# Kernel optimization log

Measured on AMD Instinct MI355X. Metric: run time of the kernel, lower is better.

## Reference

```python
import jax, jax.numpy as jnp
import numpy as np

G = 4          # deformable groups (from offset_and_mask_dim = 3*4*3*3)
K = 9          # 3x3 kernel points
GN_GROUPS = 16 # GroupNorm groups as in DyHead


def conv2d(x, w, stride=1, pad=1, groups=1):
    return jax.lax.conv_general_dilated(
        x, w, (stride, stride), [(pad, pad), (pad, pad)],
        dimension_numbers=('NCHW', 'OIHW', 'NCHW'),
        feature_group_count=groups)


def dw_conv(x, w, scale, bias):
    # YOLO Conv with g=in_channels: depthwise 3x3 + folded BN + SiLU
    C = x.shape[1]
    y = conv2d(x, w, groups=C)
    y = y * scale[None, :, None, None] + bias[None, :, None, None]
    return y * jax.nn.sigmoid(y)


def offset_mask_conv(x, w, b):
    # Conv2d(C, 108, 3, padding=1, groups=4)
    return conv2d(x, w, groups=G) + b[None, :, None, None]


def split_offset_mask(om, use_softmax):
    # om: (N,108,H,W) -> offset (N,H,W,G,K,2) in pixels (dy,dx), mask (N,H,W,G,K)
    N, _, H, W = om.shape
    om = om.transpose(0, 2, 3, 1)
    offset = om[..., :2 * G * K].reshape(N, H, W, G, K, 2)
    m = om[..., 2 * G * K:].reshape(N, H, W, G, K)
    mask = jax.nn.softmax(m, axis=-1) if use_softmax else jax.nn.sigmoid(m)
    return offset, mask


def group_norm(x, gamma, beta, eps=1e-5):
    N, C, H, W = x.shape
    xg = x.reshape(N, GN_GROUPS, C // GN_GROUPS, H, W)
    mu = xg.mean((2, 3, 4), keepdims=True)
    var = xg.var((2, 3, 4), keepdims=True)
    xg = (xg - mu) * jax.lax.rsqrt(var + eps)
    return xg.reshape(N, C, H, W) * gamma[None, :, None, None] + beta[None, :, None, None]


def dcnv3_sample(x, offset, mask, stride):
    # DCNv3 core: group-wise deformable 3x3 bilinear sampling, zero padding.
    # x: (N,C,H,W); offset: (N,Ho,Wo,G,K,2); mask: (N,Ho,Wo,G,K) -> (N,C,Ho,Wo)
    N, C, H, W = x.shape
    Cg = C // G
    Ho, Wo = offset.shape[1], offset.shape[2]
    xg = x.transpose(0, 2, 3, 1).reshape(N, H, W, G, Cg)
    kk = jnp.arange(3, dtype=x.dtype) - 1.0
    ky = jnp.repeat(kk, 3)  # (9,)
    kx = jnp.tile(kk, 3)
    base_y = (jnp.arange(Ho, dtype=x.dtype) * stride)[None, :, None, None, None]
    base_x = (jnp.arange(Wo, dtype=x.dtype) * stride)[None, None, :, None, None]
    py = base_y + ky + offset[..., 0]   # (N,Ho,Wo,G,K)
    px = base_x + kx + offset[..., 1]
    y0 = jnp.floor(py)
    x0 = jnp.floor(px)
    wy = py - y0
    wx = px - x0
    y0i = y0.astype(jnp.int32)
    x0i = x0.astype(jnp.int32)
    n_idx = jnp.arange(N)[:, None, None, None, None]
    g_idx = jnp.arange(G)[None, None, None, :, None]
    acc = jnp.zeros((N, Ho, Wo, G, Cg), x.dtype)
    for dy in (0, 1):
        for dx in (0, 1):
            yi = y0i + dy
            xi = x0i + dx
            w = (wy if dy else 1.0 - wy) * (wx if dx else 1.0 - wx)
            valid = (yi >= 0) & (yi < H) & (xi >= 0) & (xi < W)
            w = w * valid.astype(x.dtype) * mask
            v = xg[n_idx, jnp.clip(yi, 0, H - 1), jnp.clip(xi, 0, W - 1), g_idx]  # (N,Ho,Wo,G,K,Cg)
            acc = acc + jnp.einsum('nhwgk,nhwgkc->nhwgc', w, v)
    return acc.reshape(N, Ho, Wo, C).transpose(0, 3, 1, 2)


def up_bilinear_ac(x, Ho, Wo):
    # bilinear, align_corners=True
    N, C, H, W = x.shape
    def coords(out, size):
        c = jnp.arange(out, dtype=jnp.float32) * ((size - 1) / max(out - 1, 1))
        i0 = jnp.floor(c).astype(jnp.int32)
        i1 = jnp.minimum(i0 + 1, size - 1)
        return i0, i1, (c - i0).astype(x.dtype)
    y0, y1, wy = coords(Ho, H)
    xc0, xc1, wx = coords(Wo, W)
    t = x[:, :, y0, :] * (1.0 - wy)[None, None, :, None] + x[:, :, y1, :] * wy[None, None, :, None]
    return t[:, :, :, xc0] * (1.0 - wx) + t[:, :, :, xc1] * wx


def scale_attn(f, w, b):
    # AdaptiveAvgPool2d(1) -> Conv 1x1 (C->1) -> ReLU -> HSigmoid(bias=3, divisor=6)
    y = f.mean((2, 3))                      # (N,C)
    a = jax.nn.relu(y @ w.T + b)            # (N,1)
    a = jnp.clip((a + 3.0) / 6.0, 0.0, 1.0)
    return f * a[:, :, None, None]


def dyrelu(f, w1, b1_, w2, b2_):
    # DyReLU with K2=True, use_bias=True, lambda_a=2, init_a=[1,0], init_b=[0,0]
    y = f.mean((2, 3))                      # (N,C)
    h = jax.nn.relu(y @ w1.T + b1_)
    z = jnp.clip(h @ w2.T + b2_ + 3.0, 0.0, 6.0) / 6.0  # h_sigmoid
    a1, b1, a2, b2 = jnp.split(z, 4, axis=1)
    a1 = (a1 - 0.5) * 2.0 + 1.0
    a2 = (a2 - 0.5) * 2.0
    b1 = b1 - 0.5
    b2 = b2 - 0.5
    bc = lambda t: t[:, :, None, None]
    return jnp.maximum(f * bc(a1) + bc(b1), f * bc(a2) + bc(b2))


def _forward(x0, x1, x2,
             dw_w_h, dw_s_h, dw_b_h, dw_w_m, dw_s_m, dw_b_m, dw_w_l, dw_s_l, dw_b_l,
             off_w, off_b,
             gn_g_h, gn_b_h, gn_g_m, gn_b_m, gn_g_l, gn_b_l,
             sa_w, sa_b, fc1_w, fc1_b, fc2_w, fc2_b):
    xs = [x0, x1, x2]
    outs = []
    for lvl in range(3):
        x = xs[lvl]
        mid_ = dw_conv(x, dw_w_m, dw_s_m, dw_b_m)
        off, msk = split_offset_mask(offset_mask_conv(mid_, off_w, off_b), use_softmax=False)
        mid_feat = group_norm(dcnv3_sample(x, off, msk, 1), gn_g_m, gn_b_m)
        sum_feat = scale_attn(mid_feat, sa_w, sa_b)
        n_lvls = 1
        if lvl > 0:
            xl = xs[lvl - 1]
            low_ = dw_conv(xl, dw_w_l, dw_s_l, dw_b_l)
            off, msk = split_offset_mask(offset_mask_conv(low_, off_w, off_b), use_softmax=True)
            off = off[:, ::2, ::2]   # stride-2 output grid
            msk = msk[:, ::2, ::2]
            low_feat = group_norm(dcnv3_sample(xl, off, msk, 2), gn_g_l, gn_b_l)
            sum_feat = sum_feat + scale_attn(low_feat, sa_w, sa_b)
            n_lvls += 1
        if lvl < 2:
            xh = xs[lvl + 1]
            high_ = dw_conv(xh, dw_w_h, dw_s_h, dw_b_h)
            off, msk = split_offset_mask(offset_mask_conv(high_, off_w, off_b), use_softmax=True)
            high_feat = group_norm(dcnv3_sample(xh, off, msk, 1), gn_g_h, gn_b_h)
            high_feat = up_bilinear_ac(high_feat, x.shape[2], x.shape[3])
            sum_feat = sum_feat + scale_attn(high_feat, sa_w, sa_b)
            n_lvls += 1
        outs.append(dyrelu(sum_feat / n_lvls, fc1_w, fc1_b, fc2_w, fc2_b))
    return tuple(outs)


def setup_inputs() -> dict:
    key = jax.random.key(0)
    ks = jax.random.split(key, 32)
    N, C = 4, 256
    f32 = jnp.float32
    nrm = lambda k, shape, s=1.0: jax.random.normal(k, shape, f32) * s
    inp = {
        'x0': nrm(ks[0], (N, C, 80, 80)),
        'x1': nrm(ks[1], (N, C, 40, 40)),
        'x2': nrm(ks[2], (N, C, 20, 20)),
        'dw_w_h': nrm(ks[3], (C, 1, 3, 3), 0.1),
        'dw_s_h': 1.0 + nrm(ks[4], (C,), 0.1),
        'dw_b_h': nrm(ks[5], (C,), 0.1),
        'dw_w_m': nrm(ks[6], (C, 1, 3, 3), 0.1),
        'dw_s_m': 1.0 + nrm(ks[7], (C,), 0.1),
        'dw_b_m': nrm(ks[8], (C,), 0.1),
        'dw_w_l': nrm(ks[9], (C, 1, 3, 3), 0.1),
        'dw_s_l': 1.0 + nrm(ks[10], (C,), 0.1),
        'dw_b_l': nrm(ks[11], (C,), 0.1),
        'off_w': nrm(ks[12], (108, C // G, 3, 3), 0.1),
        'off_b': nrm(ks[13], (108,), 0.1),
        'gn_g_h': 1.0 + nrm(ks[14], (C,), 0.1),
        'gn_b_h': nrm(ks[15], (C,), 0.1),
        'gn_g_m': 1.0 + nrm(ks[16], (C,), 0.1),
        'gn_b_m': nrm(ks[17], (C,), 0.1),
        'gn_g_l': 1.0 + nrm(ks[18], (C,), 0.1),
        'gn_b_l': nrm(ks[19], (C,), 0.1),
        'sa_w': nrm(ks[20], (1, C), 0.05),
        'sa_b': nrm(ks[21], (1,), 0.05),
        'fc1_w': nrm(ks[22], (C // 4, C), 0.05),
        'fc1_b': nrm(ks[23], (C // 4,), 0.05),
        'fc2_w': nrm(ks[24], (4 * C, C // 4), 0.05),
        'fc2_b': nrm(ks[25], (4 * C,), 0.1),
    }
    return inp


def reference(x0, x1, x2,
              dw_w_h, dw_s_h, dw_b_h, dw_w_m, dw_s_m, dw_b_m, dw_w_l, dw_s_l, dw_b_l,
              off_w, off_b,
              gn_g_h, gn_b_h, gn_g_m, gn_b_m, gn_g_l, gn_b_l,
              sa_w, sa_b, fc1_w, fc1_b, fc2_w, fc2_b):
    return _forward(x0, x1, x2,
                    dw_w_h, dw_s_h, dw_b_h, dw_w_m, dw_s_m, dw_b_m, dw_w_l, dw_s_l, dw_b_l,
                    off_w, off_b,
                    gn_g_h, gn_b_h, gn_g_m, gn_b_m, gn_g_l, gn_b_l,
                    sa_w, sa_b, fc1_w, fc1_b, fc2_w, fc2_b)
```

## Files before the change

### kernel.cpp

```cpp
#include <hip/hip_runtime.h>
#include <hip/hip_bf16.h>

#define C_ 256
#define G_ 4

typedef __attribute__((ext_vector_type(8))) short bf16x8;
typedef __attribute__((ext_vector_type(4))) float f32x4;

static __device__ __forceinline__ unsigned short f2bf(float x) {
    __hip_bfloat16 h = __float2bfloat16(x);
    return *(unsigned short*)&h;
}
static __device__ __forceinline__ float bf2f(unsigned short u) {
    return __uint_as_float((unsigned)u << 16);
}

static __device__ __forceinline__ float upw(int y, int Hr, int Hf, float sys) {
    float inv = 1.f / sys;
    int lo = max(0, (int)((y - 1) * inv) - 1);
    int hi = min(Hf - 1, (int)((y + 1) * inv) + 1);
    float w = 0.f;
    for (int o = lo; o <= hi; o++) {
        float sy = o * sys;
        int y0 = (int)sy;
        float fy = sy - y0;
        int y1 = min(y0 + 1, Hr - 1);
        if (y0 == y) w += 1.f - fy;
        if (y1 == y) w += fy;
    }
    return w;
}

__global__ void k_prep(const float* __restrict__ off_w, const float* __restrict__ dwh,
                       const float* __restrict__ dwm, const float* __restrict__ dwl,
                       unsigned short* __restrict__ wmf, float* __restrict__ dwt,
                       float* __restrict__ zeros) {
    int i = blockIdx.x * 256 + threadIdx.x;
    const int NWM = 4 * 32 * 576;
    if (i < NWM) {
        int g = i / (32 * 576), rem = i % (32 * 576);
        int ol = rem / 576, kk = rem % 576;
        int tap = kk / 64, ic = kk % 64;
        float v = (ol < 27) ? off_w[((size_t)((g * 27 + ol) * 64 + ic)) * 9 + tap] : 0.f;
        wmf[i] = f2bf(v);
    }
    int j = i - NWM;
    if (j >= 0 && j < 3 * 2304) {
        int which = j / 2304, rem = j % 2304;
        int t = rem / 256, c = rem % 256;
        const float* src = (which == 0) ? dwh : (which == 1) ? dwm : dwl;
        dwt[j] = src[c * 9 + t];
    }
    int z = i - NWM - 3 * 2304;
    if (z >= 0 && z < 8064) zeros[z] = 0.f;
}

struct TrP {
    const float* x[3];
    unsigned short* xtb[3];
    int H[3];
    int W[3];
    int wtc[3];
    int blk[4];
};

__global__ __launch_bounds__(256) void k_transpose_b(TrP P) {
    __shared__ float tile[32][33];
    int b = blockIdx.x;
    int f = (b >= P.blk[1]) + (b >= P.blk[2]);
    int l = b - P.blk[f];
    int H = P.H[f], W = P.W[f], wtc = P.wtc[f];
    int nh = l / wtc, wtile = l - nh * wtc;
    int n = nh / H, h = nh % H;
    int w0 = wtile * 32, c0 = blockIdx.y * 32;
    const float* x = P.x[f];
    unsigned short* xtb = P.xtb[f];
    int tid = threadIdx.x;
    int i = tid / 32, j = tid % 32;
#pragma unroll
    for (int r = 0; r < 4; r++) {
        int c = c0 + i + r * 8;
        int w = w0 + j;
        tile[i + r * 8][j] = (w < W) ? x[((size_t)(n * C_ + c) * H + h) * W + w] : 0.f;
    }
    __syncthreads();
    int wj = tid >> 4, ci2 = (tid & 15) * 2;
#pragma unroll
    for (int r = 0; r < 2; r++) {
        int w = w0 + wj + r * 16;
        if (w < W) {
            ushort2 o;
            o.x = f2bf(tile[ci2][wj + r * 16]);
            o.y = f2bf(tile[ci2 + 1][wj + r * 16]);
            *(ushort2*)(xtb + ((size_t)(n * H + h) * W + w) * C_ + c0 + ci2) = o;
        }
    }
}

struct DwP {
    const unsigned short* xtb[7];
    unsigned short* out[7];
    const float* wdt[7];
    const float* sc[7];
    const float* bi[7];
    int H[7];
    int W[7];
    int blk[8];
};

__global__ __launch_bounds__(256) void k_dw_silu_b(DwP P) {
    int b = blockIdx.x;
    int f = (b >= P.blk[1]) + (b >= P.blk[2]) + (b >= P.blk[3]) + (b >= P.blk[4]) +
            (b >= P.blk[5]) + (b >= P.blk[6]);
    int H = P.H[f], W = P.W[f];
    const unsigned short* xtbf = P.xtb[f];
    unsigned short* outf = P.out[f];
    const float* wdt = P.wdt[f];
    int tid = threadIdx.x;
    int wv = tid >> 6, lane = tid & 63;
    int half = lane >> 5, l5 = lane & 31;
    int ch8 = l5 << 3;
    int pix = (b - P.blk[f]) * 8 + wv * 2 + half;
    int w = pix % W, h = (pix / W) % H, n = pix / (W * H);
    const float4 sA = *(const float4*)(P.sc[f] + ch8);
    const float4 sB = *(const float4*)(P.sc[f] + ch8 + 4);
    const float4 bA = *(const float4*)(P.bi[f] + ch8);
    const float4 bB = *(const float4*)(P.bi[f] + ch8 + 4);
    const unsigned short* xb = xtbf + (size_t)n * H * W * C_ + ch8;
    float4 accA = {0.f, 0.f, 0.f, 0.f}, accB = {0.f, 0.f, 0.f, 0.f};
#pragma unroll
    for (int t = 0; t < 9; t++) {
        int hh = h + t / 3 - 1, ww = w + t % 3 - 1;
        if (hh >= 0 && hh < H && ww >= 0 && ww < W) {
            bf16x8 xv = *(const bf16x8*)(xb + (size_t)(hh * W + ww) * C_);
            float4 wa = *(const float4*)(wdt + t * 256 + ch8);
            float4 wb = *(const float4*)(wdt + t * 256 + ch8 + 4);
            accA.x += wa.x * bf2f((unsigned short)xv[0]);
            accA.y += wa.y * bf2f((unsigned short)xv[1]);
            accA.z += wa.z * bf2f((unsigned short)xv[2]);
            accA.w += wa.w * bf2f((unsigned short)xv[3]);
            accB.x += wb.x * bf2f((unsigned short)xv[4]);
            accB.y += wb.y * bf2f((unsigned short)xv[5]);
            accB.z += wb.z * bf2f((unsigned short)xv[6]);
            accB.w += wb.w * bf2f((unsigned short)xv[7]);
        }
    }
    float y0 = accA.x * sA.x + bA.x, y1 = accA.y * sA.y + bA.y;
    float y2 = accA.z * sA.z + bA.z, y3 = accA.w * sA.w + bA.w;
    float y4 = accB.x * sB.x + bB.x, y5 = accB.y * sB.y + bB.y;
    float y6 = accB.z * sB.z + bB.z, y7 = accB.w * sB.w + bB.w;
    y0 = y0 / (1.f + __expf(-y0));
    y1 = y1 / (1.f + __expf(-y1));
    y2 = y2 / (1.f + __expf(-y2));
    y3 = y3 / (1.f + __expf(-y3));
    y4 = y4 / (1.f + __expf(-y4));
    y5 = y5 / (1.f + __expf(-y5));
    y6 = y6 / (1.f + __expf(-y6));
    y7 = y7 / (1.f + __expf(-y7));
    uint4 ov;
    ov.x = (unsigned)f2bf(y0) | ((unsigned)f2bf(y1) << 16);
    ov.y = (unsigned)f2bf(y2) | ((unsigned)f2bf(y3) << 16);
    ov.z = (unsigned)f2bf(y4) | ((unsigned)f2bf(y5) << 16);
    ov.w = (unsigned)f2bf(y6) | ((unsigned)f2bf(y7) << 16);
    *(uint4*)(outf + (size_t)pix * C_ + ch8) = ov;
}

struct OmP7 {
    const unsigned short* dwb[7];
    float* om[7];
    int Hs[7], Ws[7], Wo[7], HoWo[7];
    int ss[7];
    int ths[7], tws[7];
    int SR[7], SC[7], Msc[7];
    int nz[7], Mnz[7];
    int blk[8];
};

__global__ __launch_bounds__(256) void k_offmask_b(OmP7 P,
                                                   const unsigned short* __restrict__ wmf) {
    __shared__ __align__(16) char smem[22032];
    unsigned short* patch = (unsigned short*)smem;
    float* omv = (float*)smem;

    int tid = threadIdx.x;
    int wv = tid >> 6, lane = tid & 63;
    int n16 = lane & 15, q = lane >> 4;
    int b = blockIdx.x;
    int f = (b >= P.blk[1]) + (b >= P.blk[2]) + (b >= P.blk[3]) + (b >= P.blk[4]) +
            (b >= P.blk[5]) + (b >= P.blk[6]);
    int l = b - P.blk[f];
    int n = (l >> 2) & 3, g = l & 3;
    int tile = l >> 4;
    int nz = P.nz[f];
    int ty = (tile * P.Mnz[f]) >> 16;
    int tz = tile - ty * nz;
    int ss = P.ss[f], ths = P.ths[f], tws = P.tws[f];
    int TW = 1 << tws;
    int SR = P.SR[f], SC = P.SC[f], Msc = P.Msc[f];
    int NV = SR * SC;
    int Hs = P.Hs[f], Ws = P.Ws[f], Wo = P.Wo[f], HoWo = P.HoWo[f];
    int ho0 = ty << ths, wo0 = tz << tws;
    int hs0 = (ho0 << ss) - 1, ws0 = (wo0 << ss) - 1;
    const unsigned short* dwb = P.dwb[f];
    float* om = P.om[f];

    for (int idx = tid; idx < NV * 8; idx += 256) {
        int pp = idx >> 3;
        int c8 = (idx & 7) << 3;
        int pq = (pp * Msc) >> 16;
        int hh = hs0 + pq, ww = ws0 + (pp - pq * SC);
        uint4 v = {0u, 0u, 0u, 0u};
        if (hh >= 0 && hh < Hs && ww >= 0 && ww < Ws)
            v = *(const uint4*)(dwb + ((size_t)(n * Hs + hh) * Ws + ww) * C_ + g * 64 + c8);
        *(uint4*)(patch + pp * 72 + c8) = v;
    }
    __syncthreads();

    int bchan = q << 3;
    const unsigned short* wg = wmf + (size_t)g * 32 * 576;
    int TP = 1 << (ths + tws);
    int sc1 = SC, sc2 = SC * 2;

    if (TP == 64) {
        int p = wv * 16 + n16;
        int pr = p >> tws, pc = p & (TW - 1);
        int pixbase = (pr << ss) * SC + (pc << ss);
        f32x4 a0 = {0.f, 0.f, 0.f, 0.f}, a1 = {0.f, 0.f, 0.f, 0.f};
#pragma unroll
        for (int kk = 0; kk < 18; kk++) {
            int tap = kk >> 1;
            int ic0 = (kk & 1) << 5;
            int tr = tap / 3, tc = tap % 3;
            int ppix = pixbase + (tr == 0 ? 0 : (tr == 1 ? sc1 : sc2)) + tc;
            bf16x8 bb = *(const bf16x8*)(patch + ppix * 72 + ic0 + bchan);
            bf16x8 wa0 = *(const bf16x8*)(wg + (size_t)n16 * 576 + kk * 32 + bchan);
            bf16x8 wa1 = *(const bf16x8*)(wg + (size_t)(16 + n16) * 576 + kk * 32 + bchan);
            a0 = __builtin_amdgcn_mfma_f32_16x16x32_bf16(wa0, bb, a0, 0, 0, 0);
            a1 = __builtin_amdgcn_mfma_f32_16x16x32_bf16(wa1, bb, a1, 0, 0, 0);
        }
        __syncthreads();
#pragma unroll
        for (int r = 0; r < 4; r++) {
            int ol0 = q * 4 + r;
            omv[p * 28 + ol0] = a0[r];
            int ol1 = 16 + q * 4 + r;
            if (ol1 < 28) omv[p * 28 + ol1] = a1[r];
        }
    } else {
        int NT = TP >> 3;
        int t = wv;
        bool active = t < NT;
        int ntile = t >> 1, mtile = t & 1;
        int p = ntile * 16 + n16;
        int pr = p >> tws, pc = p & (TW - 1);
        int pixbase = (pr << ss) * SC + (pc << ss);
        f32x4 acc = {0.f, 0.f, 0.f, 0.f};
        if (active) {
#pragma unroll
            for (int kk = 0; kk < 18; kk++) {
                int tap = kk >> 1;
                int ic0 = (kk & 1) << 5;
                int tr = tap / 3, tc = tap % 3;
                int ppix = pixbase + (tr == 0 ? 0 : (tr == 1 ? sc1 : sc2)) + tc;
                bf16x8 bb = *(const bf16x8*)(patch + ppix * 72 + ic0 + bchan);
                bf16x8 wa = *(const bf16x8*)(wg + (size_t)(mtile * 16 + n16) * 576 +
                                             kk * 32 + bchan);
                acc = __builtin_amdgcn_mfma_f32_16x16x32_bf16(wa, bb, acc, 0, 0, 0);
            }
        }
        __syncthreads();
        if (active) {
#pragma unroll
            for (int r = 0; r < 4; r++) {
                int ol = mtile * 16 + q * 4 + r;
                if (ol < 28) omv[p * 28 + ol] = acc[r];
            }
        }
    }
    __syncthreads();

    float* omg = om + ((size_t)(g * 4 + n)) * HoWo * 28;
    for (int idx = tid; idx < TP * 7; idx += 256) {
        int p = (idx * 9363) >> 16;
        int c4 = idx - p * 7;
        int ho = ho0 + (p >> tws), wo = wo0 + (p & (TW - 1));
        int pixn = ho * Wo + wo;
        *(float4*)(omg + (size_t)pixn * 28 + c4 * 4) = *(float4*)(omv + p * 28 + c4 * 4);
    }
}

struct SmP {
    const unsigned short* xtb[7];
    const float* om[7];
    float* raw[7];
    float* stats[7];
    float* rsum[7];
    int Hs[7];
    int Ws[7];
    int Wo[7];
    int HoWo[7];
    int stride[7];
    int softmax[7];
    int up[7];
    int Hf[7];
    int Wf2[7];
    float sys[7];
    float sxs[7];
    int blk[8];
};

__global__ __launch_bounds__(256) void k_sample_b(SmP P, const float* __restrict__ bias) {
    int tid = threadIdx.x;
    int wv = tid >> 6, lane = tid & 63;
    int halfp = lane >> 5, l5 = lane & 31;
    int g = l5 >> 3;
    int ch8 = l5 << 3;
    int nb = gridDim.x;
    int per = nb >> 3, rem = nb & 7;
    int xcd = blockIdx.x & 7, bi = blockIdx.x >> 3;
    int logical = xcd * per + min(xcd, rem) + bi;
    int f = (logical >= P.blk[1]) + (logical >= P.blk[2]) + (logical >= P.blk[3]) +
            (logical >= P.blk[4]) + (logical >= P.blk[5]) + (logical >= P.blk[6]);
    const unsigned short* xtb = P.xtb[f];
    const float* om = P.om[f];
    float* raw = P.raw[f];
    float* stats = P.stats[f];
    float* rsum = P.rsum[f];
    int Hs = P.Hs[f], Ws = P.Ws[f], Wo = P.Wo[f], HoWo = P.HoWo[f];
    int stride = P.stride[f], softmax = P.softmax[f];
    int upf = P.up[f];
    int pix0 = (logical - P.blk[f]) * 8;
    int n = pix0 / HoWo;
    int pixn0 = pix0 - n * HoWo;

    __shared__ float lom[8 * 112];
    __shared__ float lb[108];
    __shared__ float sm[32][9];
    __shared__ float4 lw[288];
    __shared__ ushort4 li[288];
    __shared__ float lstat[32];
    __shared__ float lsum[8][256];
    __shared__ float wup[8];

    if (tid < 224) {
        int gc = tid / 56, r2 = tid % 56;
        int pp = r2 / 7, c4 = r2 % 7;
        float4 v = *(const float4*)(om + ((size_t)(gc * 4 + n) * HoWo + pixn0 + pp) * 28 +
                                    c4 * 4);
        ((float4*)lom)[pp * 28 + gc * 7 + c4] = v;
    }
    if (tid < 108) lb[tid] = bias[tid];
    if (tid < 32) lstat[tid] = 0.f;
    __syncthreads();

    if (tid < 32) {
        int pp = tid >> 2, gs = tid & 3;
        float mv[9];
#pragma unroll
        for (int k = 0; k < 9; k++) {
            int ch = 72 + gs * 9 + k;
            int gc = ch / 27;
            mv[k] = lom[pp * 112 + gc * 28 + (ch - gc * 27)] + lb[ch];
        }
        if (softmax) {
            float mx = -1e30f;
#pragma unroll
            for (int k = 0; k < 9; k++) mx = fmaxf(mx, mv[k]);
            float ssum = 0.f;
#pragma unroll
            for (int k = 0; k < 9; k++) {
                mv[k] = __expf(mv[k] - mx);
                ssum += mv[k];
            }
            float inv = 1.f / ssum;
#pragma unroll
            for (int k = 0; k < 9; k++) sm[tid][k] = mv[k] * inv;
        } else {
#pragma unroll
            for (int k = 0; k < 9; k++) sm[tid][k] = 1.f / (1.f + __expf(-mv[k]));
        }
    }
    if (tid < 8) {
        float w = 1.f;
        if (upf) {
            int Ho = HoWo / Wo;
            int pixn = pixn0 + tid;
            int ho = pixn / Wo, wo = pixn - ho * Wo;
            w = upw(ho, Ho, P.Hf[f], P.sys[f]) * upw(wo, Wo, P.Wf2[f], P.sxs[f]);
        }
        wup[tid] = w;
    }
    __syncthreads();

    for (int idx = tid; idx < 288; idx += 256) {
        int pg = idx / 9, k = idx % 9;
        int pp = pg >> 2, gs = pg & 3;
        int chy = gs * 18 + 2 * k, chx = chy + 1;
        int gcy = chy / 27, gcx = chx / 27;
        float oy = lom[pp * 112 + gcy * 28 + (chy - gcy * 27)] + lb[chy];
        float ox = lom[pp * 112 + gcx * 28 + (chx - gcx * 27)] + lb[chx];
        int pixn = pixn0 + pp;
        int ho = pixn / Wo, wo = pixn % Wo;
        float py = (float)(ho * stride + k / 3 - 1) + oy;
        float px = (float)(wo * stride + k % 3 - 1) + ox;
        float y0f = floorf(py), x0f = floorf(px);
        int y0 = (int)y0f, x0 = (int)x0f;
        float wy = py - y0f, wx = px - x0f;
        int y1 = y0 + 1, x1 = x0 + 1;
        float v0y = (y0 >= 0 && y0 < Hs) ? 1.f : 0.f;
        float v1y = (y1 >= 0 && y1 < Hs) ? 1.f : 0.f;
        float v0x = (x0 >= 0 && x0 < Ws) ? 1.f : 0.f;
        float v1x = (x1 >= 0 && x1 < Ws) ? 1.f : 0.f;
        int y0c = min(max(y0, 0), Hs - 1), y1c = min(max(y1, 0), Hs - 1);
        int x0c = min(max(x0, 0), Ws - 1), x1c = min(max(x1, 0), Ws - 1);
        float m_ = sm[pg][k];
        float4 w4;
        w4.x = (1.f - wy) * (1.f - wx) * v0y * v0x * m_;
        w4.y = (1.f - wy) * wx * v0y * v1x * m_;
        w4.z = wy * (1.f - wx) * v1y * v0x * m_;
        w4.w = wy * wx * v1y * v1x * m_;
        ushort4 i4;
        i4.x = (unsigned short)(y0c * Ws + x0c);
        i4.y = (unsigned short)(y0c * Ws + x1c);
        i4.z = (unsigned short)(y1c * Ws + x0c);
        i4.w = (unsigned short)(y1c * Ws + x1c);
        lw[pp * 36 + gs * 9 + k] = w4;
        li[pp * 36 + gs * 9 + k] = i4;
    }
    __syncthreads();

    int px = wv * 2 + halfp;
    const unsigned short* xb = xtb + (size_t)n * Hs * Ws * C_ + ch8;
    float4 aL = {0.f, 0.f, 0.f, 0.f}, aH = {0.f, 0.f, 0.f, 0.f};
#pragma unroll
    for (int k = 0; k < 9; k++) {
        float4 w4 = lw[px * 36 + g * 9 + k];
        ushort4 i4 = li[px * 36 + g * 9 + k];
        bf16x8 v0 = *(const bf16x8*)(xb + ((size_t)i4.x << 8));
        bf16x8 v1 = *(const bf16x8*)(xb + ((size_t)i4.y << 8));
        bf16x8 v2 = *(const bf16x8*)(xb + ((size_t)i4.z << 8));
        bf16x8 v3 = *(const bf16x8*)(xb + ((size_t)i4.w << 8));
        aL.x += w4.x * bf2f((unsigned short)v0[0]) + w4.y * bf2f((unsigned short)v1[0]) +
                w4.z * bf2f((unsigned short)v2[0]) + w4.w * bf2f((unsigned short)v3[0]);
        aL.y += w4.x * bf2f((unsigned short)v0[1]) + w4.y * bf2f((unsigned short)v1[1]) +
                w4.z * bf2f((unsigned short)v2[1]) + w4.w * bf2f((unsigned short)v3[1]);
        aL.z += w4.x * bf2f((unsigned short)v0[2]) + w4.y * bf2f((unsigned short)v1[2]) +
                w4.z * bf2f((unsigned short)v2[2]) + w4.w * bf2f((unsigned short)v3[2]);
        aL.w += w4.x * bf2f((unsigned short)v0[3]) + w4.y * bf2f((unsigned short)v1[3]) +
                w4.z * bf2f((unsigned short)v2[3]) + w4.w * bf2f((unsigned short)v3[3]);
        aH.x += w4.x * bf2f((unsigned short)v0[4]) + w4.y * bf2f((unsigned short)v1[4]) +
                w4.z * bf2f((unsigned short)v2[4]) + w4.w * bf2f((unsigned short)v3[4]);
        aH.y += w4.x * bf2f((unsigned short)v0[5]) + w4.y * bf2f((unsigned short)v1[5]) +
                w4.z * bf2f((unsigned short)v2[5]) + w4.w * bf2f((unsigned short)v3[5]);
        aH.z += w4.x * bf2f((unsigned short)v0[6]) + w4.y * bf2f((unsigned short)v1[6]) +
                w4.z * bf2f((unsigned short)v2[6]) + w4.w * bf2f((unsigned short)v3[6]);
        aH.w += w4.x * bf2f((unsigned short)v0[7]) + w4.y * bf2f((unsigned short)v1[7]) +
                w4.z * bf2f((unsigned short)v2[7]) + w4.w * bf2f((unsigned short)v3[7]);
    }
    *(float4*)(raw + (size_t)(pix0 + px) * C_ + ch8) = aL;
    *(float4*)(raw + (size_t)(pix0 + px) * C_ + ch8 + 4) = aH;
    *(float4*)&lsum[px][ch8] = aL;
    *(float4*)&lsum[px][ch8 + 4] = aH;
    float gs = aL.x + aL.y + aL.z + aL.w + aH.x + aH.y + aH.z + aH.w;
    float gss = aL.x * aL.x + aL.y * aL.y + aL.z * aL.z + aL.w * aL.w + aH.x * aH.x +
                aH.y * aH.y + aH.z * aH.z + aH.w * aH.w;
    gs += __shfl_down(gs, 1, 2);
    gss += __shfl_down(gss, 1, 2);
    if ((lane & 1) == 0) {
        atomicAdd(&lstat[(l5 >> 1) * 2 + 0], gs);
        atomicAdd(&lstat[(l5 >> 1) * 2 + 1], gss);
    }
    __syncthreads();
    if (tid < 32) atomicAdd(&stats[n * 32 + tid], lstat[tid]);
    {
        float s = 0.f;
#pragma unroll
        for (int p2 = 0; p2 < 8; p2++) s += wup[p2] * lsum[p2][tid];
        atomicAdd(&rsum[n * 256 + tid], s);
    }
}

struct CfF {
    const float* rsum;
    const float* stats;
    const float* gamma;
    const float* beta;
    float cnt;
};
struct CfP {
    CfF ft[3][3];
    int nf[3];
    float inv_nl[3];
    float inv_hw[3];
};

__global__ __launch_bounds__(256) void k_coef_b(CfP P,
                                                const float* __restrict__ sa_w,
                                                const float* __restrict__ sa_b,
                                                const float* __restrict__ fc1_w,
                                                const float* __restrict__ fc1_b,
                                                const float* __restrict__ fc2_w,
                                                const float* __restrict__ fc2_b,
                                                float* __restrict__ coef,
                                                float* __restrict__ af) {
    int lvl = blockIdx.x >> 2;
    int n = blockIdx.x & 3;
    int nf = P.nf[lvl];
    float inv_nl = P.inv_nl[lvl], inv_hw = P.inv_hw[lvl];
    int c = threadIdx.x;
    __shared__ float red[256];
    __shared__ float meanv[256];
    __shared__ float hv[64];
    __shared__ float sa_a[3];
    float cm[3] = {0.f, 0.f, 0.f};
    int gg = c >> 4;
    for (int f = 0; f < nf; f++) {
        CfF s = P.ft[lvl][f];
        float s1 = s.stats[(n * 16 + gg) * 2], s2 = s.stats[(n * 16 + gg) * 2 + 1];
        float mu = s1 / s.cnt;
        float var = s2 / s.cnt - mu * mu;
        float rs = rsqrtf(var + 1e-5f);
        float ga = s.gamma[c] * rs;
        float be = s.beta[c] - mu * ga;
        cm[f] = ga * s.rsum[n * 256 + c] * inv_hw + be;
        red[c] = sa_w[c] * cm[f];
        __syncthreads();
        for (int st = 128; st; st >>= 1) {
            if (c < st) red[c] += red[c + st];
            __syncthreads();
        }
        if (c == 0) {
            float t = fmaxf(red[0] + sa_b[0], 0.f);
            sa_a[f] = fminf(fmaxf((t + 3.f) * (1.f / 6.f), 0.f), 1.f);
        }
        __syncthreads();
    }
    float mv = 0.f;
    for (int f = 0; f < nf; f++) mv += sa_a[f] * cm[f];
    mv *= inv_nl;
    meanv[c] = mv;
    __syncthreads();
    int j = c >> 2, t = c & 3;
    float partial = 0.f;
    for (int k = t * 64; k < t * 64 + 64; k++) partial += fc1_w[j * 256 + k] * meanv[k];
    partial += __shfl_down(partial, 2, 4);
    partial += __shfl_down(partial, 1, 4);
    if (t == 0) hv[j] = fmaxf(partial + fc1_b[j], 0.f);
    __syncthreads();
    float zz[4];
#pragma unroll
    for (int i = 0; i < 4; i++) {
        float z = fc2_b[i * 256 + c];
        for (int k = 0; k < 64; k++) z += fc2_w[(size_t)(i * 256 + c) * 64 + k] * hv[k];
        zz[i] = fminf(fmaxf(z + 3.f, 0.f), 6.f) * (1.f / 6.f);
    }
    float* cf = coef + lvl * 4096;
    cf[n * 1024 + 0 * 256 + c] = (zz[0] - 0.5f) * 2.f + 1.f;
    cf[n * 1024 + 1 * 256 + c] = zz[1] - 0.5f;
    cf[n * 1024 + 2 * 256 + c] = (zz[2] - 0.5f) * 2.f;
    cf[n * 1024 + 3 * 256 + c] = zz[3] - 0.5f;
    if (c < 4) af[lvl * 16 + n * 4 + c] = (c < nf) ? sa_a[c] * inv_nl : 0.f;
}

struct StF {
    const float* raw;
    const float* stats;
    const float* gamma;
    const float* beta;
    float cnt;
    int up;
    int Hr;
    int Wr;
    float sys;
    float sxs;
};
struct StP {
    StF ft[3][3];
    float* out[3];
    int nf[3];
    int HW[3];
    int Wf[3];
    int npt[3];
    int blk[4];
};

__global__ __launch_bounds__(256) void k_store_b(StP P, const float* __restrict__ coef,
                                                 const float* __restrict__ af) {
    __shared__ float tile[64][65];
    int b = blockIdx.x;
    int f = (b >= P.blk[1]) + (b >= P.blk[2]);
    int l = b - P.blk[f];
    int npt = P.npt[f], HW = P.HW[f], Wf = P.Wf[f], nf = P.nf[f];
    int n = l / (npt * 4);
    int r_ = l - n * (npt * 4);
    int pt = r_ >> 2;
    int c0 = (r_ & 3) * 64;
    float* out = P.out[f];
    const float* coefL = coef + f * 4096;
    const float* afL = af + f * 16;
    int tid = threadIdx.x;
    int lane16 = tid & 15, prow = tid >> 4;
    int ch4 = c0 + lane16 * 4;
    int gg = ch4 >> 4;
    float a0 = afL[n * 4 + 0], a1f = afL[n * 4 + 1], a2f = afL[n * 4 + 2];
    float4 ca1 = *(const float4*)(coefL + n * 1024 + 0 + ch4);
    float4 cb1 = *(const float4*)(coefL + n * 1024 + 256 + ch4);
    float4 ca2 = *(const float4*)(coefL + n * 1024 + 512 + ch4);
    float4 cb2 = *(const float4*)(coefL + n * 1024 + 768 + ch4);

    StF sA = P.ft[f][0], sB = P.ft[f][1], sC = P.ft[f][2];
    auto mkgb = [&](const StF& s, float4& ga, float4& be) {
        float s1 = s.stats[(n * 16 + gg) * 2], s2 = s.stats[(n * 16 + gg) * 2 + 1];
        float mu = s1 / s.cnt;
        float var = s2 / s.cnt - mu * mu;
        float rs = rsqrtf(var + 1e-5f);
        float4 gm = *(const float4*)(s.gamma + ch4);
        float4 bt = *(const float4*)(s.beta + ch4);
        ga.x = gm.x * rs; be.x = bt.x - mu * ga.x;
        ga.y = gm.y * rs; be.y = bt.y - mu * ga.y;
        ga.z = gm.z * rs; be.z = bt.z - mu * ga.z;
        ga.w = gm.w * rs; be.w = bt.w - mu * ga.w;
    };
    float4 gaA, beA, gaB, beB, gaC = {0, 0, 0, 0}, beC = {0, 0, 0, 0};
    mkgb(sA, gaA, beA);
    mkgb(sB, gaB, beB);
    if (nf > 2) mkgb(sC, gaC, beC);

    auto rdf = [&](const StF& s, int p) -> float4 {
        if (!s.up) return *(const float4*)(s.raw + ((size_t)n * HW + p) * C_ + ch4);
        int ho = p / Wf, wo = p - ho * Wf;
        float sy = ho * s.sys, sx = wo * s.sxs;
        int y0 = (int)sy, x0 = (int)sx;
        float fy = sy - y0, fx = sx - x0;
        int y1 = min(y0 + 1, s.Hr - 1), x1 = min(x0 + 1, s.Wr - 1);
        const float* rb = s.raw + (size_t)n * s.Hr * s.Wr * C_ + ch4;
        float4 v00 = *(const float4*)(rb + (size_t)(y0 * s.Wr + x0) * C_);
        float4 v01 = *(const float4*)(rb + (size_t)(y0 * s.Wr + x1) * C_);
        float4 v10 = *(const float4*)(rb + (size_t)(y1 * s.Wr + x0) * C_);
        float4 v11 = *(const float4*)(rb + (size_t)(y1 * s.Wr + x1) * C_);
        float4 v;
        v.x = (v00.x * (1.f - fy) + v10.x * fy) * (1.f - fx) + (v01.x * (1.f - fy) + v11.x * fy) * fx;
        v.y = (v00.y * (1.f - fy) + v10.y * fy) * (1.f - fx) + (v01.y * (1.f - fy) + v11.y * fy) * fx;
        v.z = (v00.z * (1.f - fy) + v10.z * fy) * (1.f - fx) + (v01.z * (1.f - fy) + v11.z * fy) * fx;
        v.w = (v00.w * (1.f - fy) + v10.w * fy) * (1.f - fx) + (v01.w * (1.f - fy) + v11.w * fy) * fx;
        return v;
    };

#pragma unroll
    for (int pass = 0; pass < 4; pass++) {
        int px = pass * 16 + prow;
        int p = pt * 64 + px;
        if (p < HW) {
            float4 vA = rdf(sA, p);
            float4 fv;
            fv.x = (vA.x * gaA.x + beA.x) * a0;
            fv.y = (vA.y * gaA.y + beA.y) * a0;
            fv.z = (vA.z * gaA.z + beA.z) * a0;
            fv.w = (vA.w * gaA.w + beA.w) * a0;
            float4 vB = rdf(sB, p);
            fv.x += (vB.x * gaB.x + beB.x) * a1f;
            fv.y += (vB.y * gaB.y + beB.y) * a1f;
            fv.z += (vB.z * gaB.z + beB.z) * a1f;
            fv.w += (vB.w * gaB.w + beB.w) * a1f;
            if (nf > 2) {
                float4 vC = rdf(sC, p);
                fv.x += (vC.x * gaC.x + beC.x) * a2f;
                fv.y += (vC.y * gaC.y + beC.y) * a2f;
                fv.z += (vC.z * gaC.z + beC.z) * a2f;
                fv.w += (vC.w * gaC.w + beC.w) * a2f;
            }
            int cr = lane16 * 4;
            tile[cr + 0][px] = fmaxf(fv.x * ca1.x + cb1.x, fv.x * ca2.x + cb2.x);
            tile[cr + 1][px] = fmaxf(fv.y * ca1.y + cb1.y, fv.y * ca2.y + cb2.y);
            tile[cr + 2][px] = fmaxf(fv.z * ca1.z + cb1.z, fv.z * ca2.z + cb2.z);
            tile[cr + 3][px] = fmaxf(fv.w * ca1.w + cb1.w, fv.w * ca2.w + cb2.w);
        }
    }
    __syncthreads();
#pragma unroll
    for (int wp = 0; wp < 4; wp++) {
        int row = wp * 16 + (tid >> 4);
        int px4 = (tid & 15) * 4;
        int p = pt * 64 + px4;
        if (p < HW) {
            float4 r;
            r.x = tile[row][px4 + 0];
            r.y = tile[row][px4 + 1];
            r.z = tile[row][px4 + 2];
            r.w = tile[row][px4 + 3];
            *(float4*)(out + (size_t)(n * C_ + c0 + row) * HW + p) = r;
        }
    }
}

extern "C" void kernel_launch(void* const* d_in, const int* in_sizes, int n_in,
                              void* d_out, int out_size, void* d_ws, size_t ws_size,
                              hipStream_t stream) {
    (void)in_sizes; (void)n_in; (void)out_size; (void)ws_size;
    const float* x0 = (const float*)d_in[0];
    const float* x1 = (const float*)d_in[1];
    const float* x2 = (const float*)d_in[2];
    const float* dw_w_h = (const float*)d_in[3];
    const float* dw_s_h = (const float*)d_in[4];
    const float* dw_b_h = (const float*)d_in[5];
    const float* dw_w_m = (const float*)d_in[6];
    const float* dw_s_m = (const float*)d_in[7];
    const float* dw_b_m = (const float*)d_in[8];
    const float* dw_w_l = (const float*)d_in[9];
    const float* dw_s_l = (const float*)d_in[10];
    const float* dw_b_l = (const float*)d_in[11];
    const float* off_w = (const float*)d_in[12];
    const float* off_b = (const float*)d_in[13];
    const float* gn_g_h = (const float*)d_in[14];
    const float* gn_b_h = (const float*)d_in[15];
    const float* gn_g_m = (const float*)d_in[16];
    const float* gn_b_m = (const float*)d_in[17];
    const float* gn_g_l = (const float*)d_in[18];
    const float* gn_b_l = (const float*)d_in[19];
    const float* sa_w = (const float*)d_in[20];
    const float* sa_b = (const float*)d_in[21];
    const float* fc1_w = (const float*)d_in[22];
    const float* fc1_b = (const float*)d_in[23];
    const float* fc2_w = (const float*)d_in[24];
    const float* fc2_b = (const float*)d_in[25];

    float* ws = (float*)d_ws;
    unsigned short* XTB0 = (unsigned short*)(ws + 0);
    unsigned short* XTB1 = (unsigned short*)(ws + 3276800);
    unsigned short* XTB2 = (unsigned short*)(ws + 4096000);
    float* SH = ws + 4300800;
    float* FINA = ws + 10854400;
    float* FINB = ws + 17408000;
    float* FINC = ws + 23961600;
    float* WMF = ws + 25600000;
    float* DWT = ws + 25636864;
    float* STATS = ws + 25643776;
    float* RAWSUM = ws + 25644672;

    unsigned short* SHB = (unsigned short*)SH;
    unsigned short* FINAB = (unsigned short*)FINA;
    unsigned short* WMFB = (unsigned short*)WMF;

    float* out0 = (float*)d_out;
    float* out1 = out0 + 6553600;
    float* out2 = out0 + 8192000;

    float* OM_l0mid = out0;
    float* OM_l0high = out0 + 2867200;
    float* OM_l1mid = out0 + 3584000;
    float* OM_l1low = out0 + 4300800;
    float* OM_l1high = out1;
    float* OM_l2mid = out1 + 179200;
    float* OM_l2low = out1 + 358400;

    float* RAW_l0mid = SH;
    float* RAW_l0high = FINC;
    float* RAW_l1mid = FINB;
    float* RAW_l1low = FINB + 1638400;
    float* RAW_l1high = FINB + 3276800;
    float* RAW_l2mid = FINB + 3686400;
    float* RAW_l2low = FINB + 4096000;
    float* COEF = FINA;
    float* AF = FINA + 12288;

    const float SYS_L0H = (float)(39.0 / 79.0);
    const float SYS_L1H = (float)(19.0 / 39.0);

    k_prep<<<(4 * 32 * 576 + 6912 + 8064 + 255) / 256, 256, 0, stream>>>(
        off_w, dw_w_h, dw_w_m, dw_w_l, WMFB, DWT, STATS);

    {
        TrP tp{};
        tp.x[0] = x0; tp.xtb[0] = XTB0; tp.H[0] = 80; tp.W[0] = 80; tp.wtc[0] = 3;
        tp.x[1] = x1; tp.xtb[1] = XTB1; tp.H[1] = 40; tp.W[1] = 40; tp.wtc[1] = 2;
        tp.x[2] = x2; tp.xtb[2] = XTB2; tp.H[2] = 20; tp.W[2] = 20; tp.wtc[2] = 1;
        tp.blk[0] = 0; tp.blk[1] = 960; tp.blk[2] = 1280; tp.blk[3] = 1360;
        k_transpose_b<<<dim3(1360, 8), 256, 0, stream>>>(tp);
    }

    unsigned short* DWB_x0mid = SHB;
    unsigned short* DWB_x0low = SHB + 6553600;
    unsigned short* DWB_x1high = FINAB;
    unsigned short* DWB_x1mid = FINAB + 1638400;
    unsigned short* DWB_x1low = FINAB + 3276800;
    unsigned short* DWB_x2high = FINAB + 4915200;
    unsigned short* DWB_x2mid = FINAB + 5324800;

    {
        DwP dp{};
        dp.xtb[0] = XTB0; dp.out[0] = DWB_x0mid;  dp.wdt[0] = DWT + 1 * 2304;
        dp.sc[0] = dw_s_m; dp.bi[0] = dw_b_m; dp.H[0] = 80; dp.W[0] = 80;
        dp.xtb[1] = XTB0; dp.out[1] = DWB_x0low;  dp.wdt[1] = DWT + 2 * 2304;
        dp.sc[1] = dw_s_l; dp.bi[1] = dw_b_l; dp.H[1] = 80; dp.W[1] = 80;
        dp.xtb[2] = XTB1; dp.out[2] = DWB_x1high; dp.wdt[2] = DWT + 0 * 2304;
        dp.sc[2] = dw_s_h; dp.bi[2] = dw_b_h; dp.H[2] = 40; dp.W[2] = 40;
        dp.xtb[3] = XTB1; dp.out[3] = DWB_x1mid;  dp.wdt[3] = DWT + 1 * 2304;
        dp.sc[3] = dw_s_m; dp.bi[3] = dw_b_m; dp.H[3] = 40; dp.W[3] = 40;
        dp.xtb[4] = XTB1; dp.out[4] = DWB_x1low;  dp.wdt[4] = DWT + 2 * 2304;
        dp.sc[4] = dw_s_l; dp.bi[4] = dw_b_l; dp.H[4] = 40; dp.W[4] = 40;
        dp.xtb[5] = XTB2; dp.out[5] = DWB_x2high; dp.wdt[5] = DWT + 0 * 2304;
        dp.sc[5] = dw_s_h; dp.bi[5] = dw_b_h; dp.H[5] = 20; dp.W[5] = 20;
        dp.xtb[6] = XTB2; dp.out[6] = DWB_x2mid;  dp.wdt[6] = DWT + 1 * 2304;
        dp.sc[6] = dw_s_m; dp.bi[6] = dw_b_m; dp.H[6] = 20; dp.W[6] = 20;
        dp.blk[0] = 0;    dp.blk[1] = 3200; dp.blk[2] = 6400; dp.blk[3] = 7200;
        dp.blk[4] = 8000; dp.blk[5] = 8800; dp.blk[6] = 9000; dp.blk[7] = 9200;
        k_dw_silu_b<<<9200, 256, 0, stream>>>(dp);
    }

    {
        OmP7 op{};
        auto setf = [&](int i, const unsigned short* dwb, float* om, int Hs, int Ws,
                        int Wo, int HoWo, int ss, int ths, int tws, int SR, int SC,
                        int nz) {
            op.dwb[i] = dwb; op.om[i] = om;
            op.Hs[i] = Hs; op.Ws[i] = Ws; op.Wo[i] = Wo; op.HoWo[i] = HoWo;
            op.ss[i] = ss; op.ths[i] = ths; op.tws[i] = tws;
            op.SR[i] = SR; op.SC[i] = SC; op.Msc[i] = (65536 + SC - 1) / SC;
            op.nz[i] = nz; op.Mnz[i] = (65536 + nz - 1) / nz;
        };
        setf(0, DWB_x0mid,  OM_l0mid,  80, 80, 80, 6400, 0, 3, 3, 10, 10, 10);
        setf(1, DWB_x1high, OM_l0high, 40, 40, 40, 1600, 0, 2, 3, 6,  10, 5);
        setf(2, DWB_x1mid,  OM_l1mid,  40, 40, 40, 1600, 0, 2, 3, 6,  10, 5);
        setf(3, DWB_x0low,  OM_l1low,  80, 80, 40, 1600, 1, 2, 3, 9,  17, 5);
        setf(4, DWB_x2high, OM_l1high, 20, 20, 20, 400,  0, 2, 2, 6,  6,  5);
        setf(5, DWB_x2mid,  OM_l2mid,  20, 20, 20, 400,  0, 2, 2, 6,  6,  5);
        setf(6, DWB_x1low,  OM_l2low,  40, 40, 20, 400,  1, 2, 2, 9,  9,  5);
        op.blk[0] = 0;    op.blk[1] = 1600; op.blk[2] = 2400; op.blk[3] = 3200;
        op.blk[4] = 4000; op.blk[5] = 4400; op.blk[6] = 4800; op.blk[7] = 5200;
        k_offmask_b<<<5200, 256, 0, stream>>>(op, WMFB);
    }

    {
        SmP sp{};
        auto setf = [&](int i, const unsigned short* xtb, const float* om, float* raw,
                        int slot, int Hs, int Ws, int Wo, int HoWo, int stride,
                        int softmax, int up, int Hf, int Wf2, float sys, float sxs) {
            sp.xtb[i] = xtb; sp.om[i] = om; sp.raw[i] = raw;
            sp.stats[i] = STATS + slot * 128;
            sp.rsum[i] = RAWSUM + slot * 1024;
            sp.Hs[i] = Hs; sp.Ws[i] = Ws; sp.Wo[i] = Wo; sp.HoWo[i] = HoWo;
            sp.stride[i] = stride; sp.softmax[i] = softmax;
            sp.up[i] = up; sp.Hf[i] = Hf; sp.Wf2[i] = Wf2;
            sp.sys[i] = sys; sp.sxs[i] = sxs;
        };
        setf(0, XTB0, OM_l0mid,  RAW_l0mid,  0, 80, 80, 80, 6400, 1, 0, 0, 80, 80, 1.f, 1.f);
        setf(1, XTB1, OM_l0high, RAW_l0high, 1, 40, 40, 40, 1600, 1, 1, 1, 80, 80, SYS_L0H, SYS_L0H);
        setf(2, XTB1, OM_l1mid,  RAW_l1mid,  2, 40, 40, 40, 1600, 1, 0, 0, 40, 40, 1.f, 1.f);
        setf(3, XTB0, OM_l1low,  RAW_l1low,  3, 80, 80, 40, 1600, 2, 1, 0, 40, 40, 1.f, 1.f);
        setf(4, XTB2, OM_l1high, RAW_l1high, 4, 20, 20, 20, 400,  1, 1, 1, 40, 40, SYS_L1H, SYS_L1H);
        setf(5, XTB2, OM_l2mid,  RAW_l2mid,  5, 20, 20, 20, 400,  1, 0, 0, 20, 20, 1.f, 1.f);
        setf(6, XTB1, OM_l2low,  RAW_l2low,  6, 40, 40, 20, 400,  2, 1, 0, 20, 20, 1.f, 1.f);
        sp.blk[0] = 0;    sp.blk[1] = 3200; sp.blk[2] = 4000; sp.blk[3] = 4800;
        sp.blk[4] = 5600; sp.blk[5] = 5800; sp.blk[6] = 6000; sp.blk[7] = 6200;
        k_sample_b<<<6200, 256, 0, stream>>>(sp, off_b);
    }

    {
        CfP cp{};
        cp.nf[0] = 2; cp.inv_nl[0] = 0.5f;      cp.inv_hw[0] = 1.f / 6400.f;
        cp.nf[1] = 3; cp.inv_nl[1] = 1.f / 3.f; cp.inv_hw[1] = 1.f / 1600.f;
        cp.nf[2] = 2; cp.inv_nl[2] = 0.5f;      cp.inv_hw[2] = 1.f / 400.f;
        cp.ft[0][0] = {RAWSUM + 0 * 1024, STATS + 0 * 128, gn_g_m, gn_b_m, 102400.f};
        cp.ft[0][1] = {RAWSUM + 1 * 1024, STATS + 1 * 128, gn_g_h, gn_b_h, 25600.f};
        cp.ft[1][0] = {RAWSUM + 2 * 1024, STATS + 2 * 128, gn_g_m, gn_b_m, 25600.f};
        cp.ft[1][1] = {RAWSUM + 3 * 1024, STATS + 3 * 128, gn_g_l, gn_b_l, 25600.f};
        cp.ft[1][2] = {RAWSUM + 4 * 1024, STATS + 4 * 128, gn_g_h, gn_b_h, 6400.f};
        cp.ft[2][0] = {RAWSUM + 5 * 1024, STATS + 5 * 128, gn_g_m, gn_b_m, 6400.f};
        cp.ft[2][1] = {RAWSUM + 6 * 1024, STATS + 6 * 128, gn_g_l, gn_b_l, 6400.f};
        k_coef_b<<<12, 256, 0, stream>>>(cp, sa_w, sa_b, fc1_w, fc1_b, fc2_w, fc2_b,
                                         COEF, AF);
    }

    {
        StP st{};
        st.out[0] = out0; st.nf[0] = 2; st.HW[0] = 6400; st.Wf[0] = 80; st.npt[0] = 100;
        st.out[1] = out1; st.nf[1] = 3; st.HW[1] = 1600; st.Wf[1] = 40; st.npt[1] = 25;
        st.out[2] = out2; st.nf[2] = 2; st.HW[2] = 400;  st.Wf[2] = 20; st.npt[2] = 7;
        st.ft[0][0] = {RAW_l0mid,  STATS + 0 * 128, gn_g_m, gn_b_m, 102400.f, 0, 80, 80, 1.f, 1.f};
        st.ft[0][1] = {RAW_l0high, STATS + 1 * 128, gn_g_h, gn_b_h, 25600.f,  1, 40, 40, SYS_L0H, SYS_L0H};
        st.ft[1][0] = {RAW_l1mid,  STATS + 2 * 128, gn_g_m, gn_b_m, 25600.f,  0, 40, 40, 1.f, 1.f};
        st.ft[1][1] = {RAW_l1low,  STATS + 3 * 128, gn_g_l, gn_b_l, 25600.f,  0, 40, 40, 1.f, 1.f};
        st.ft[1][2] = {RAW_l1high, STATS + 4 * 128, gn_g_h, gn_b_h, 6400.f,   1, 20, 20, SYS_L1H, SYS_L1H};
        st.ft[2][0] = {RAW_l2mid,  STATS + 5 * 128, gn_g_m, gn_b_m, 6400.f,   0, 20, 20, 1.f, 1.f};
        st.ft[2][1] = {RAW_l2low,  STATS + 6 * 128, gn_g_l, gn_b_l, 6400.f,   0, 20, 20, 1.f, 1.f};
        st.blk[0] = 0; st.blk[1] = 1600; st.blk[2] = 2000; st.blk[3] = 2112;
        k_store_b<<<2112, 256, 0, stream>>>(st, COEF, AF);
    }
}
```

Measured before the change: 357.6 us.

## Store sampled features as bf16, replicate reduction sums, vectorize coef matvecs

The deformable-sampling kernel now writes its raw per-pixel outputs as bf16 instead of fp32, which halves write traffic and halves the read traffic in the store kernel that consumes them. The per-channel upsample-weighted sum atomics are spread across 4 replicated buffers indexed by block id to reduce atomic contention, and the coef kernel adds the replicas back together. The small FC matvecs in the coef kernel use float4 loads. Rounding the intermediates to bf16 adds error before GroupNorm is applied.

```diff
diff --git a/kernel.cpp b/kernel.cpp
--- a/kernel.cpp
+++ b/kernel.cpp
@@ -13,6 +13,14 @@
 }
 static __device__ __forceinline__ float bf2f(unsigned short u) {
     return __uint_as_float((unsigned)u << 16);
+}
+static __device__ __forceinline__ float4 bf4(ushort4 u) {
+    float4 r;
+    r.x = bf2f(u.x);
+    r.y = bf2f(u.y);
+    r.z = bf2f(u.z);
+    r.w = bf2f(u.w);
+    return r;
 }
 
 static __device__ __forceinline__ float upw(int y, int Hr, int Hf, float sys) {
@@ -34,7 +42,7 @@
 __global__ void k_prep(const float* __restrict__ off_w, const float* __restrict__ dwh,
                        const float* __restrict__ dwm, const float* __restrict__ dwl,
                        unsigned short* __restrict__ wmf, float* __restrict__ dwt,
-                       float* __restrict__ zeros) {
+                       float* __restrict__ zeros, float* __restrict__ rep) {
     int i = blockIdx.x * 256 + threadIdx.x;
     const int NWM = 4 * 32 * 576;
     if (i < NWM) {
@@ -52,7 +60,9 @@
         dwt[j] = src[c * 9 + t];
     }
     int z = i - NWM - 3 * 2304;
-    if (z >= 0 && z < 8064) zeros[z] = 0.f;
+    if (z >= 0 && z < 896) zeros[z] = 0.f;
+    int z2 = z - 896;
+    if (z2 >= 0 && z2 < 4 * 7168) rep[z2] = 0.f;
 }
 
 struct TrP {
@@ -292,7 +302,7 @@
 struct SmP {
     const unsigned short* xtb[7];
     const float* om[7];
-    float* raw[7];
+    unsigned short* raw[7];
     float* stats[7];
     float* rsum[7];
     int Hs[7];
@@ -323,9 +333,9 @@
             (logical >= P.blk[4]) + (logical >= P.blk[5]) + (logical >= P.blk[6]);
     const unsigned short* xtb = P.xtb[f];
     const float* om = P.om[f];
-    float* raw = P.raw[f];
+    unsigned short* raw = P.raw[f];
     float* stats = P.stats[f];
-    float* rsum = P.rsum[f];
+    float* rsum = P.rsum[f] + (blockIdx.x & 3) * 7168;
     int Hs = P.Hs[f], Ws = P.Ws[f], Wo = P.Wo[f], HoWo = P.HoWo[f];
     int stride = P.stride[f], softmax = P.softmax[f];
     int upf = P.up[f];
@@ -457,8 +467,12 @@
         aH.w += w4.x * bf2f((unsigned short)v0[7]) + w4.y * bf2f((unsigned short)v1[7]) +
                 w4.z * bf2f((unsigned short)v2[7]) + w4.w * bf2f((unsigned short)v3[7]);
     }
-    *(float4*)(raw + (size_t)(pix0 + px) * C_ + ch8) = aL;
-    *(float4*)(raw + (size_t)(pix0 + px) * C_ + ch8 + 4) = aH;
+    uint4 ov;
+    ov.x = (unsigned)f2bf(aL.x) | ((unsigned)f2bf(aL.y) << 16);
+    ov.y = (unsigned)f2bf(aL.z) | ((unsigned)f2bf(aL.w) << 16);
+    ov.z = (unsigned)f2bf(aH.x) | ((unsigned)f2bf(aH.y) << 16);
+    ov.w = (unsigned)f2bf(aH.z) | ((unsigned)f2bf(aH.w) << 16);
+    *(uint4*)(raw + (size_t)(pix0 + px) * C_ + ch8) = ov;
     *(float4*)&lsum[px][ch8] = aL;
     *(float4*)&lsum[px][ch8 + 4] = aH;
     float gs = aL.x + aL.y + aL.z + aL.w + aH.x + aH.y + aH.z + aH.w;
@@ -509,8 +523,8 @@
     float inv_nl = P.inv_nl[lvl], inv_hw = P.inv_hw[lvl];
     int c = threadIdx.x;
     __shared__ float red[256];
-    __shared__ float meanv[256];
-    __shared__ float hv[64];
+    __shared__ __align__(16) float meanv[256];
+    __shared__ __align__(16) float hv[64];
     __shared__ float sa_a[3];
     float cm[3] = {0.f, 0.f, 0.f};
     int gg = c >> 4;
@@ -522,7 +536,9 @@
         float rs = rsqrtf(var + 1e-5f);
         float ga = s.gamma[c] * rs;
         float be = s.beta[c] - mu * ga;
-        cm[f] = ga * s.rsum[n * 256 + c] * inv_hw + be;
+        float wsum = s.rsum[0 * 7168 + n * 256 + c] + s.rsum[1 * 7168 + n * 256 + c] +
+                     s.rsum[2 * 7168 + n * 256 + c] + s.rsum[3 * 7168 + n * 256 + c];
+        cm[f] = ga * wsum * inv_hw + be;
         red[c] = sa_w[c] * cm[f];
         __syncthreads();
         for (int st = 128; st; st >>= 1) {
@@ -542,7 +558,15 @@
     __syncthreads();
     int j = c >> 2, t = c & 3;
     float partial = 0.f;
-    for (int k = t * 64; k < t * 64 + 64; k++) partial += fc1_w[j * 256 + k] * meanv[k];
+    {
+        const float4* fw = (const float4*)(fc1_w + j * 256 + t * 64);
+        const float4* mv4 = (const float4*)(meanv + t * 64);
+#pragma unroll
+        for (int kk = 0; kk < 16; kk++) {
+            float4 a = fw[kk], bb = mv4[kk];
+            partial += a.x * bb.x + a.y * bb.y + a.z * bb.z + a.w * bb.w;
+        }
+    }
     partial += __shfl_down(partial, 2, 4);
     partial += __shfl_down(partial, 1, 4);
     if (t == 0) hv[j] = fmaxf(partial + fc1_b[j], 0.f);
@@ -551,7 +575,13 @@
 #pragma unroll
     for (int i = 0; i < 4; i++) {
         float z = fc2_b[i * 256 + c];
-        for (int k = 0; k < 64; k++) z += fc2_w[(size_t)(i * 256 + c) * 64 + k] * hv[k];
+        const float4* f2 = (const float4*)(fc2_w + (size_t)(i * 256 + c) * 64);
+        const float4* h4 = (const float4*)hv;
+#pragma unroll
+        for (int kk = 0; kk < 16; kk++) {
+            float4 a = f2[kk], bb = h4[kk];
+            z += a.x * bb.x + a.y * bb.y + a.z * bb.z + a.w * bb.w;
+        }
         zz[i] = fminf(fmaxf(z + 3.f, 0.f), 6.f) * (1.f / 6.f);
     }
     float* cf = coef + lvl * 4096;
@@ -563,7 +593,7 @@
 }
 
 struct StF {
-    const float* raw;
+    const unsigned short* raw;
     const float* stats;
     const float* gamma;
     const float* beta;
@@ -627,17 +657,18 @@
     if (nf > 2) mkgb(sC, gaC, beC);
 
     auto rdf = [&](const StF& s, int p) -> float4 {
-        if (!s.up) return *(const float4*)(s.raw + ((size_t)n * HW + p) * C_ + ch4);
+        if (!s.up)
+            return bf4(*(const ushort4*)(s.raw + ((size_t)n * HW + p) * C_ + ch4));
         int ho = p / Wf, wo = p - ho * Wf;
         float sy = ho * s.sys, sx = wo * s.sxs;
         int y0 = (int)sy, x0 = (int)sx;
         float fy = sy - y0, fx = sx - x0;
         int y1 = min(y0 + 1, s.Hr - 1), x1 = min(x0 + 1, s.Wr - 1);
-        const float* rb = s.raw + (size_t)n * s.Hr * s.Wr * C_ + ch4;
-        float4 v00 = *(const float4*)(rb + (size_t)(y0 * s.Wr + x0) * C_);
-        float4 v01 = *(const float4*)(rb + (size_t)(y0 * s.Wr + x1) * C_);
-        float4 v10 = *(const float4*)(rb + (size_t)(y1 * s.Wr + x0) * C_);
-        float4 v11 = *(const float4*)(rb + (size_t)(y1 * s.Wr + x1) * C_);
+        const unsigned short* rb = s.raw + (size_t)n * s.Hr * s.Wr * C_ + ch4;
+        float4 v00 = bf4(*(const ushort4*)(rb + (size_t)(y0 * s.Wr + x0) * C_));
+        float4 v01 = bf4(*(const ushort4*)(rb + (size_t)(y0 * s.Wr + x1) * C_));
+        float4 v10 = bf4(*(const ushort4*)(rb + (size_t)(y1 * s.Wr + x0) * C_));
+        float4 v11 = bf4(*(const ushort4*)(rb + (size_t)(y1 * s.Wr + x1) * C_));
         float4 v;
         v.x = (v00.x * (1.f - fy) + v10.x * fy) * (1.f - fx) + (v01.x * (1.f - fy) + v11.x * fy) * fx;
         v.y = (v00.y * (1.f - fy) + v10.y * fy) * (1.f - fx) + (v01.y * (1.f - fy) + v11.y * fy) * fx;
@@ -735,7 +766,6 @@
     float* WMF = ws + 25600000;
     float* DWT = ws + 25636864;
     float* STATS = ws + 25643776;
-    float* RAWSUM = ws + 25644672;
 
     unsigned short* SHB = (unsigned short*)SH;
     unsigned short* FINAB = (unsigned short*)FINA;
@@ -753,21 +783,22 @@
     float* OM_l2mid = out1 + 179200;
     float* OM_l2low = out1 + 358400;
 
-    float* RAW_l0mid = SH;
-    float* RAW_l0high = FINC;
-    float* RAW_l1mid = FINB;
-    float* RAW_l1low = FINB + 1638400;
-    float* RAW_l1high = FINB + 3276800;
-    float* RAW_l2mid = FINB + 3686400;
-    float* RAW_l2low = FINB + 4096000;
+    unsigned short* RAW_l0mid = (unsigned short*)SH;
+    unsigned short* RAW_l0high = (unsigned short*)FINC;
+    unsigned short* RAW_l1mid = (unsigned short*)FINB;
+    unsigned short* RAW_l1low = (unsigned short*)(FINB + 1638400);
+    unsigned short* RAW_l1high = (unsigned short*)(FINB + 3276800);
+    unsigned short* RAW_l2mid = (unsigned short*)(FINB + 3686400);
+    unsigned short* RAW_l2low = (unsigned short*)(FINB + 4096000);
+    float* REP = FINB + 4505600;
     float* COEF = FINA;
     float* AF = FINA + 12288;
 
     const float SYS_L0H = (float)(39.0 / 79.0);
     const float SYS_L1H = (float)(19.0 / 39.0);
 
-    k_prep<<<(4 * 32 * 576 + 6912 + 8064 + 255) / 256, 256, 0, stream>>>(
-        off_w, dw_w_h, dw_w_m, dw_w_l, WMFB, DWT, STATS);
+    k_prep<<<(4 * 32 * 576 + 6912 + 896 + 28672 + 255) / 256, 256, 0, stream>>>(
+        off_w, dw_w_h, dw_w_m, dw_w_l, WMFB, DWT, STATS, REP);
 
     {
         TrP tp{};
@@ -832,12 +863,13 @@
 
     {
         SmP sp{};
-        auto setf = [&](int i, const unsigned short* xtb, const float* om, float* raw,
-                        int slot, int Hs, int Ws, int Wo, int HoWo, int stride,
-                        int softmax, int up, int Hf, int Wf2, float sys, float sxs) {
+        auto setf = [&](int i, const unsigned short* xtb, const float* om,
+                        unsigned short* raw, int slot, int Hs, int Ws, int Wo, int HoWo,
+                        int stride, int softmax, int up, int Hf, int Wf2, float sys,
+                        float sxs) {
             sp.xtb[i] = xtb; sp.om[i] = om; sp.raw[i] = raw;
             sp.stats[i] = STATS + slot * 128;
-            sp.rsum[i] = RAWSUM + slot * 1024;
+            sp.rsum[i] = REP + slot * 1024;
             sp.Hs[i] = Hs; sp.Ws[i] = Ws; sp.Wo[i] = Wo; sp.HoWo[i] = HoWo;
             sp.stride[i] = stride; sp.softmax[i] = softmax;
             sp.up[i] = up; sp.Hf[i] = Hf; sp.Wf2[i] = Wf2;
@@ -860,13 +892,13 @@
         cp.nf[0] = 2; cp.inv_nl[0] = 0.5f;      cp.inv_hw[0] = 1.f / 6400.f;
         cp.nf[1] = 3; cp.inv_nl[1] = 1.f / 3.f; cp.inv_hw[1] = 1.f / 1600.f;
         cp.nf[2] = 2; cp.inv_nl[2] = 0.5f;      cp.inv_hw[2] = 1.f / 400.f;
-        cp.ft[0][0] = {RAWSUM + 0 * 1024, STATS + 0 * 128, gn_g_m, gn_b_m, 102400.f};
-        cp.ft[0][1] = {RAWSUM + 1 * 1024, STATS + 1 * 128, gn_g_h, gn_b_h, 25600.f};
-        cp.ft[1][0] = {RAWSUM + 2 * 1024, STATS + 2 * 128, gn_g_m, gn_b_m, 25600.f};
-        cp.ft[1][1] = {RAWSUM + 3 * 1024, STATS + 3 * 128, gn_g_l, gn_b_l, 25600.f};
-        cp.ft[1][2] = {RAWSUM + 4 * 1024, STATS + 4 * 128, gn_g_h, gn_b_h, 6400.f};
-        cp.ft[2][0] = {RAWSUM + 5 * 1024, STATS + 5 * 128, gn_g_m, gn_b_m, 6400.f};
-        cp.ft[2][1] = {RAWSUM + 6 * 1024, STATS + 6 * 128, gn_g_l, gn_b_l, 6400.f};
+        cp.ft[0][0] = {REP + 0 * 1024, STATS + 0 * 128, gn_g_m, gn_b_m, 102400.f};
+        cp.ft[0][1] = {REP + 1 * 1024, STATS + 1 * 128, gn_g_h, gn_b_h, 25600.f};
+        cp.ft[1][0] = {REP + 2 * 1024, STATS + 2 * 128, gn_g_m, gn_b_m, 25600.f};
+        cp.ft[1][1] = {REP + 3 * 1024, STATS + 3 * 128, gn_g_l, gn_b_l, 25600.f};
+        cp.ft[1][2] = {REP + 4 * 1024, STATS + 4 * 128, gn_g_h, gn_b_h, 6400.f};
+        cp.ft[2][0] = {REP + 5 * 1024, STATS + 5 * 128, gn_g_m, gn_b_m, 6400.f};
+        cp.ft[2][1] = {REP + 6 * 1024, STATS + 6 * 128, gn_g_l, gn_b_l, 6400.f};
         k_coef_b<<<12, 256, 0, stream>>>(cp, sa_w, sa_b, fc1_w, fc1_b, fc2_w, fc2_b,
                                          COEF, AF);
     }
```

Result: no change. 358.6 us (+0.3%).
